# Kernel tuning notes

Measured on AMD Instinct MI355X. Metric: run time of the kernel, lower is better.

Reference implementation:

```python
import jax, jax.numpy as jnp
import numpy as np

B, S, N_NODES, D_IN = 8, 24, 400, 3
D_MODEL = 32
G1_HEADS, G1_DIM = 4, 16
G2_HEADS, G2_DIM = 1, 32
T_KEY = 32


def _ln(x, g, b, eps=1e-6):
    m = jnp.mean(x, -1, keepdims=True)
    v = jnp.var(x, -1, keepdims=True)
    return g * (x - m) / jnp.sqrt(v + eps) + b


def _gat(x, adj, wq, bq, wk, bk, wv, bv, heads, dim):
    # x: [B*, N, F]; adjacency-masked multi-head attention (GraphAttention)
    Bx, N, _ = x.shape
    q = (x @ wq + bq).reshape(Bx, N, heads, dim)
    k = (x @ wk + bk).reshape(Bx, N, heads, dim)
    v = (x @ wv + bv).reshape(Bx, N, heads, dim)
    s = jnp.einsum('bihd,bjhd->bhij', q, k) / jnp.sqrt(jnp.float32(dim))
    s = jnp.where((adj == 0)[None, None], jnp.float32(-1e9), s)
    w = jax.nn.softmax(s, axis=-1)
    o = jnp.einsum('bhij,bjhd->bihd', w, v)
    return o.reshape(Bx, N, heads * dim)


def _mha(x, wq, bq, wk, bk, wv, bv, wo, bo):
    # keras MultiHeadAttention(num_heads=2, key_dim=32), self-attention, output dim = 32
    q = jnp.einsum('bsd,dhk->bshk', x, wq) + bq
    k = jnp.einsum('bsd,dhk->bshk', x, wk) + bk
    v = jnp.einsum('bsd,dhk->bshk', x, wv) + bv
    a = jax.nn.softmax(jnp.einsum('bqhk,bshk->bhqs', q, k) / jnp.sqrt(jnp.float32(T_KEY)), axis=-1)
    o = jnp.einsum('bhqs,bshk->bqhk', a, v)
    return jnp.einsum('bqhk,hko->bqo', o, wo) + bo


def setup_inputs() -> dict:
    ks = jax.random.split(jax.random.key(0), 20)

    def w(k, shape, scale=0.05):
        return (jax.random.normal(k, shape) * scale).astype(jnp.float32)

    z = lambda *s: jnp.zeros(s, jnp.float32)
    one = lambda *s: jnp.ones(s, jnp.float32)

    d = {}
    d['inputs'] = jax.random.normal(ks[0], (B, S, N_NODES, D_IN), dtype=jnp.float32)
    adj = (jax.random.uniform(ks[1], (N_NODES, N_NODES)) < 0.05).astype(jnp.float32)
    adj = jnp.minimum(adj + jnp.eye(N_NODES, dtype=jnp.float32), 1.0)
    d['adj'] = adj / (jnp.sum(adj, axis=1, keepdims=True) + 1e-6)  # row-normalized

    d['g1_wq'] = w(ks[2], (D_IN, G1_HEADS * G1_DIM)); d['g1_bq'] = z(G1_HEADS * G1_DIM)
    d['g1_wk'] = w(ks[3], (D_IN, G1_HEADS * G1_DIM)); d['g1_bk'] = z(G1_HEADS * G1_DIM)
    d['g1_wv'] = w(ks[4], (D_IN, G1_HEADS * G1_DIM)); d['g1_bv'] = z(G1_HEADS * G1_DIM)
    d['g2_wq'] = w(ks[5], (G1_HEADS * G1_DIM, G2_DIM)); d['g2_bq'] = z(G2_DIM)
    d['g2_wk'] = w(ks[6], (G1_HEADS * G1_DIM, G2_DIM)); d['g2_bk'] = z(G2_DIM)
    d['g2_wv'] = w(ks[7], (G1_HEADS * G1_DIM, G2_DIM)); d['g2_bv'] = z(G2_DIM)
    d['sp_g'] = one(D_MODEL); d['sp_b'] = z(D_MODEL)
    d['t_wq'] = w(ks[8], (D_MODEL, 2, T_KEY)); d['t_bq'] = z(2, T_KEY)
    d['t_wk'] = w(ks[9], (D_MODEL, 2, T_KEY)); d['t_bk'] = z(2, T_KEY)
    d['t_wv'] = w(ks[10], (D_MODEL, 2, T_KEY)); d['t_bv'] = z(2, T_KEY)
    d['t_wo'] = w(ks[11], (2, T_KEY, D_MODEL)); d['t_bo'] = z(D_MODEL)
    d['ff_w1'] = w(ks[12], (D_MODEL, 64)); d['ff_b1'] = z(64)
    d['ff_w2'] = w(ks[13], (64, D_MODEL)); d['ff_b2'] = z(D_MODEL)
    d['ln1_g'] = one(D_MODEL); d['ln1_b'] = z(D_MODEL)
    d['ln2_g'] = one(D_MODEL); d['ln2_b'] = z(D_MODEL)
    d['fin_g'] = one(D_MODEL); d['fin_b'] = z(D_MODEL)
    d['fd_w'] = w(ks[14], (D_MODEL, 1), scale=0.01); d['fd_b'] = z(1)
    return d


def reference(inputs, adj, g1_wq, g1_bq, g1_wk, g1_bk, g1_wv, g1_bv,
              g2_wq, g2_bq, g2_wk, g2_bk, g2_wv, g2_bv, sp_g, sp_b,
              t_wq, t_bq, t_wk, t_bk, t_wv, t_bv, t_wo, t_bo,
              ff_w1, ff_b1, ff_w2, ff_b2, ln1_g, ln1_b, ln2_g, ln2_b,
              fin_g, fin_b, fd_w, fd_b):
    Bx, Sx, N, _ = inputs.shape
    x = inputs.reshape(Bx * Sx, N, D_IN)

    # SpatialProcessor: GAT1 -> relu -> GAT2 -> residual layernorm
    h = jax.nn.relu(_gat(x, adj, g1_wq, g1_bq, g1_wk, g1_bk, g1_wv, g1_bv, G1_HEADS, G1_DIM))
    h = _gat(h, adj, g2_wq, g2_bq, g2_wk, g2_bk, g2_wv, g2_bv, G2_HEADS, G2_DIM)
    res = jnp.pad(x, ((0, 0), (0, 0), (0, D_MODEL - D_IN)))  # zero-pad 3 -> 32 for residual
    sp = _ln(h + res, sp_g, sp_b)
    sp4 = sp.reshape(Bx, Sx, N, D_MODEL)  # [B, S, N, 32]

    # TemporalTransformer over sequence per node
    t_in = jnp.transpose(sp4, (0, 2, 1, 3)).reshape(Bx * N, Sx, D_MODEL)
    a = _mha(t_in, t_wq, t_bq, t_wk, t_bk, t_wv, t_bv, t_wo, t_bo)
    x1 = _ln(t_in + a, ln1_g, ln1_b)
    f = jax.nn.gelu(x1 @ ff_w1 + ff_b1, approximate=False) @ ff_w2 + ff_b2
    t_out = _ln(x1 + f, ln2_g, ln2_b).reshape(Bx, N, Sx, D_MODEL)

    # fuse: mean over seq (spatial) + mean over seq (temporal), layernorm, final dense
    fused = _ln(jnp.mean(sp4, axis=1) + jnp.mean(t_out, axis=2), fin_g, fin_b)
    return (fused @ fd_w + fd_b)[..., 0]  # [B, N]
```

## Files before the change

kernel.cpp:

```cpp
#include <hip/hip_runtime.h>
#include <hip/hip_bf16.h>

#define NN 400
#define KMAX 64

struct PtrTable {
  const void* p[36];
  int off[37];
};

__device__ __forceinline__ float bflo(unsigned u) {
  union { unsigned i; float f; } x; x.i = u << 16; return x.f;
}
__device__ __forceinline__ float bfhi(unsigned u) {
  union { unsigned i; float f; } x; x.i = u & 0xffff0000u; return x.f;
}
__device__ __forceinline__ unsigned short f2bf(float f) {
  __hip_bfloat16 b = __float2bfloat16(f);
  return *reinterpret_cast<unsigned short*>(&b);
}
__device__ __forceinline__ unsigned packbf(float a, float b) {
  return (unsigned)f2bf(a) | ((unsigned)f2bf(b) << 16);
}

__global__ void detect_dtype_k(const unsigned short* __restrict__ probe,
                               int* __restrict__ flag) {
  int lane = threadIdx.x;
  unsigned short u = probe[lane * 2];
  int e = (u >> 7) & 0xFF;
  bool plaus = (u == 0) || (e >= 112 && e <= 132);
  unsigned long long m = __ballot(plaus);
  if (lane == 0) flag[0] = (__popcll(m) >= 48) ? 1 : 0;
}

__global__ void convert_k(PtrTable pt, const int* __restrict__ flag,
                          float* __restrict__ dst) {
  bool isbf = flag[0] != 0;
  int total = pt.off[36];
  for (int i = blockIdx.x * blockDim.x + threadIdx.x; i < total;
       i += gridDim.x * blockDim.x) {
    int lo = 0, hi = 35;
    while (lo < hi) {
      int mid = (lo + hi + 1) >> 1;
      if (i >= pt.off[mid]) lo = mid; else hi = mid - 1;
    }
    int rel = i - pt.off[lo];
    float v;
    if (isbf) v = __bfloat162float(((const __hip_bfloat16*)pt.p[lo])[rel]);
    else      v = ((const float*)pt.p[lo])[rel];
    dst[i] = v;
  }
}

__global__ void build_csr_k(const float* __restrict__ adj,
                            int* __restrict__ colp, int* __restrict__ degp) {
  int row = blockIdx.x, lane = threadIdx.x;
  int base = 0;
  for (int j0 = 0; j0 < NN; j0 += 64) {
    int j = j0 + lane;
    bool nz = (j < NN) && (adj[row * NN + j] != 0.0f);
    unsigned long long m = __ballot(nz);
    int offl = __popcll(m & ((1ull << lane) - 1ull));
    if (nz) {
      int pidx = base + offl;
      if (pidx < KMAX) colp[row * KMAX + pidx] = j;
    }
    base += __popcll(m);
  }
  if (lane == 0) degp[row] = base < KMAX ? base : KMAX;
}

__global__ __launch_bounds__(256) void gat1_k(
    const float* __restrict__ xin, const float* __restrict__ g1,
    const int* __restrict__ colp, const int* __restrict__ degp,
    unsigned short* __restrict__ h1b) {
  __shared__ float xs[NN * 3];
  __shared__ float w1s[768];
  __shared__ unsigned short kb[NN * 18];
  __shared__ unsigned short vb[NN * 18];
  const int tid = threadIdx.x;
  const int g = blockIdx.x, co = blockIdx.y * 16;
  for (int e = tid; e < NN * 3; e += 256) xs[e] = xin[g * NN * 3 + e];
  for (int e = tid; e < 768; e += 256) w1s[e] = g1[e];
  __syncthreads();
  for (int e = tid; e < NN * 16; e += 256) {
    int n = e >> 4, c = e & 15;
    float x0 = xs[n * 3], x1 = xs[n * 3 + 1], x2 = xs[n * 3 + 2];
    int wc = co + c;
    float kk = w1s[448 + wc] + x0 * w1s[256 + wc] + x1 * w1s[320 + wc] + x2 * w1s[384 + wc];
    float vv = w1s[704 + wc] + x0 * w1s[512 + wc] + x1 * w1s[576 + wc] + x2 * w1s[640 + wc];
    kb[n * 18 + c] = f2bf(kk);
    vb[n * 18 + c] = f2bf(vv);
  }
  __syncthreads();
  for (int i = tid; i < NN; i += 256) {
    float x0 = xs[i * 3], x1 = xs[i * 3 + 1], x2 = xs[i * 3 + 2];
    float q[16], o[16];
    #pragma unroll
    for (int c = 0; c < 16; ++c) {
      int wc = co + c;
      q[c] = w1s[192 + wc] + x0 * w1s[wc] + x1 * w1s[64 + wc] + x2 * w1s[128 + wc];
      o[c] = 0.f;
    }
    int dg = degp[i];
    const int* cols = colp + i * KMAX;
    float l = 0.f;
    for (int e = 0; e < dg; ++e) {
      int j = cols[e];
      const unsigned* kr = (const unsigned*)(kb + j * 18);
      const unsigned* vr = (const unsigned*)(vb + j * 18);
      float s = 0.f;
      #pragma unroll
      for (int c = 0; c < 8; ++c) {
        unsigned u = kr[c];
        s += q[2 * c] * bflo(u) + q[2 * c + 1] * bfhi(u);
      }
      float p = __expf(s * 0.25f);
      l += p;
      #pragma unroll
      for (int c = 0; c < 8; ++c) {
        unsigned u = vr[c];
        o[2 * c]     += p * bflo(u);
        o[2 * c + 1] += p * bfhi(u);
      }
    }
    float inv = 1.f / l;
    unsigned* hr = (unsigned*)(h1b + ((size_t)g * NN + i) * 64 + co);
    #pragma unroll
    for (int c = 0; c < 8; ++c)
      hr[c] = packbf(fmaxf(o[2 * c] * inv, 0.f), fmaxf(o[2 * c + 1] * inv, 0.f));
  }
}

__global__ __launch_bounds__(256) void gat2_proj_k(
    const unsigned short* __restrict__ h1b, const float* __restrict__ g2,
    unsigned short* __restrict__ q2b, unsigned short* __restrict__ k2g,
    unsigned short* __restrict__ v2g) {
  __shared__ float ht[64 * 65];
  __shared__ float wqs[2048], wks[2048], wvs[2048];
  __shared__ float bqs[32], bks[32], bvs[32];
  const int tid = threadIdx.x, t = blockIdx.x;
  for (int e = tid; e < 2048; e += 256) {
    unsigned u = ((const unsigned*)h1b)[t * 2048 + e];
    int ln = e >> 5, d = (e & 31) * 2;
    ht[ln * 65 + d] = bflo(u);
    ht[ln * 65 + d + 1] = bfhi(u);
  }
  for (int e = tid; e < 2048; e += 256) {
    wqs[e] = g2[e]; wks[e] = g2[2080 + e]; wvs[e] = g2[4160 + e];
  }
  if (tid < 32) { bqs[tid] = g2[2048 + tid]; bks[tid] = g2[4128 + tid]; bvs[tid] = g2[6208 + tid]; }
  __syncthreads();
  const int c = tid & 31, ng = tid >> 5;
  float qa[8], ka[8], va[8];
  #pragma unroll
  for (int k = 0; k < 8; ++k) { qa[k] = bqs[c]; ka[k] = bks[c]; va[k] = bvs[c]; }
  for (int d = 0; d < 64; ++d) {
    float wq = wqs[d * 32 + c], wk = wks[d * 32 + c], wv = wvs[d * 32 + c];
    #pragma unroll
    for (int k = 0; k < 8; ++k) {
      float hv = ht[(ng * 8 + k) * 65 + d];
      qa[k] += hv * wq; ka[k] += hv * wk; va[k] += hv * wv;
    }
  }
  #pragma unroll
  for (int k = 0; k < 8; ++k) {
    int gn = t * 64 + ng * 8 + k;
    q2b[gn * 32 + c] = f2bf(qa[k]);
    k2g[gn * 32 + c] = f2bf(ka[k]);
    v2g[gn * 32 + c] = f2bf(va[k]);
  }
}

__global__ __launch_bounds__(256) void gat2_attn_k(
    const float* __restrict__ xin, const unsigned short* __restrict__ q2b,
    const unsigned short* __restrict__ k2g, const unsigned short* __restrict__ v2g,
    const float* __restrict__ spw, const int* __restrict__ colp,
    const int* __restrict__ degp, float* __restrict__ spo) {
  __shared__ unsigned short k2s[NN * 34];
  __shared__ unsigned short v2s[NN * 34];
  __shared__ float gw[64];
  const int tid = threadIdx.x;
  const int g = blockIdx.x;
  if (tid < 64) gw[tid] = spw[tid];
  for (int e = tid; e < 6400; e += 256) {
    unsigned uk = ((const unsigned*)k2g)[g * 6400 + e];
    unsigned uv = ((const unsigned*)v2g)[g * 6400 + e];
    int n = e >> 4, c = (e & 15) * 2;
    *(unsigned*)(k2s + n * 34 + c) = uk;
    *(unsigned*)(v2s + n * 34 + c) = uv;
  }
  __syncthreads();
  const int b = g / 24, st = g % 24;
  const int i0 = blockIdx.y * 200;
  for (int i = i0 + tid; i < i0 + 200; i += 256) {
    const unsigned* qr = (const unsigned*)(q2b + ((size_t)g * NN + i) * 32);
    float q[32], o[32];
    #pragma unroll
    for (int c = 0; c < 16; ++c) {
      unsigned u = qr[c];
      q[2 * c] = bflo(u); q[2 * c + 1] = bfhi(u);
      o[2 * c] = 0.f; o[2 * c + 1] = 0.f;
    }
    int dg = degp[i];
    const int* cols = colp + i * KMAX;
    float l = 0.f;
    for (int e = 0; e < dg; ++e) {
      int j = cols[e];
      const unsigned* kr = (const unsigned*)(k2s + j * 34);
      float s = 0.f;
      #pragma unroll
      for (int c = 0; c < 16; ++c) {
        unsigned u = kr[c];
        s += q[2 * c] * bflo(u) + q[2 * c + 1] * bfhi(u);
      }
      float p = __expf(s * 0.17677669529663688f);
      l += p;
      const unsigned* vr = (const unsigned*)(v2s + j * 34);
      #pragma unroll
      for (int c = 0; c < 16; ++c) {
        unsigned u = vr[c];
        o[2 * c]     += p * bflo(u);
        o[2 * c + 1] += p * bfhi(u);
      }
    }
    float inv = 1.f / l;
    const float* xr = xin + ((size_t)g * NN + i) * 3;
    float row[32];
    #pragma unroll
    for (int c = 0; c < 32; ++c) row[c] = o[c] * inv;
    row[0] += xr[0]; row[1] += xr[1]; row[2] += xr[2];
    float mean = 0.f;
    #pragma unroll
    for (int c = 0; c < 32; ++c) mean += row[c];
    mean *= (1.f / 32.f);
    float var = 0.f;
    #pragma unroll
    for (int c = 0; c < 32; ++c) { float dd = row[c] - mean; var += dd * dd; }
    var *= (1.f / 32.f);
    float rinv = 1.f / sqrtf(var + 1e-6f);
    float* so = spo + (((size_t)b * NN + i) * 24 + st) * 32;
    float4* so4 = (float4*)so;
    #pragma unroll
    for (int k = 0; k < 8; ++k) {
      float4 v;
      v.x = gw[4 * k]     * (row[4 * k]     - mean) * rinv + gw[32 + 4 * k];
      v.y = gw[4 * k + 1] * (row[4 * k + 1] - mean) * rinv + gw[33 + 4 * k];
      v.z = gw[4 * k + 2] * (row[4 * k + 2] - mean) * rinv + gw[34 + 4 * k];
      v.w = gw[4 * k + 3] * (row[4 * k + 3] - mean) * rinv + gw[35 + 4 * k];
      so4[k] = v;
    }
  }
}

__global__ __launch_bounds__(128) void temporal_k(
    const float* __restrict__ sp, const float* __restrict__ tw,
    const int* __restrict__ flag, void* __restrict__ outp) {
  __shared__ float sm[7472];
  float* t_s = sm;
  float* q_s = sm + 768;
  float* k_s = sm + 2328;
  float* v_s = sm + 3888;
  float* aw  = sm + 5448;
  float* x1s = sm + 6648;
  float* red = sm + 7440;
  float* att = q_s;
  float* f1s = k_s;
  float* tos = v_s;
  const int tid = threadIdx.x;

  const float* twq = tw;            const float* tbq = tw + 2048;
  const float* twk = tw + 2112;     const float* tbk = tw + 4160;
  const float* twv = tw + 4224;     const float* tbv = tw + 6272;
  const float* two = tw + 6336;     const float* tbo = tw + 8384;
  const float* fw1 = tw + 8416;     const float* fb1 = tw + 10464;
  const float* fw2 = tw + 10528;    const float* fb2 = tw + 12576;
  const float* l1g = tw + 12608;    const float* l1b = tw + 12640;
  const float* l2g = tw + 12672;    const float* l2b = tw + 12704;
  const float* fng = tw + 12736;    const float* fnb = tw + 12768;
  const float* fdw = tw + 12800;    const float* fdb = tw + 12832;

  const float4* base4 = (const float4*)(sp + (size_t)blockIdx.x * 768);
  for (int e = tid; e < 192; e += 128) ((float4*)t_s)[e] = base4[e];
  __syncthreads();

  {
    const int hk = tid & 63, sh = tid >> 6;
    for (int a = 0; a < 3; ++a) {
      const float* W  = (a == 0) ? twq : (a == 1) ? twk : twv;
      const float* Bb = (a == 0) ? tbq : (a == 1) ? tbk : tbv;
      float* dst      = (a == 0) ? q_s : (a == 1) ? k_s : v_s;
      float w[32];
      #pragma unroll
      for (int c = 0; c < 32; ++c) w[c] = W[c * 64 + hk];
      float bias = Bb[hk];
      for (int s = sh * 12; s < sh * 12 + 12; ++s) {
        float acc = bias;
        const float* tr = t_s + s * 32;
        #pragma unroll
        for (int c = 0; c < 32; ++c) acc += tr[c] * w[c];
        dst[s * 65 + hk] = acc;
      }
    }
  }
  __syncthreads();

  if (tid < 96) {
    const int h = tid / 48, rem = tid % 48, qs = rem >> 1, half = rem & 1;
    const float* qr = q_s + qs * 65 + h * 32;
    float sc[12], l = 0.f;
    #pragma unroll
    for (int k = 0; k < 12; ++k) {
      const float* kr = k_s + (half * 12 + k) * 65 + h * 32;
      float s = 0.f;
      #pragma unroll
      for (int d = 0; d < 32; ++d) s += qr[d] * kr[d];
      sc[k] = __expf(s * 0.17677669529663688f);
      l += sc[k];
    }
    l += __shfl_xor(l, 1);
    float inv = 1.f / l;
    float* ar = aw + (h * 24 + qs) * 25 + half * 12;
    #pragma unroll
    for (int k = 0; k < 12; ++k) ar[k] = sc[k] * inv;
  }
  __syncthreads();

  for (int e = tid; e < 1536; e += 128) {
    int qs = e >> 6, hk = e & 63, h = hk >> 5;
    const float* ar = aw + (h * 24 + qs) * 25;
    float a = 0.f;
    #pragma unroll
    for (int ss = 0; ss < 24; ++ss) a += ar[ss] * v_s[ss * 65 + hk];
    att[qs * 65 + hk] = a;
  }
  __syncthreads();

  for (int e = tid; e < 768; e += 128) {
    int s = e >> 5, c = e & 31;
    const float* ar = att + s * 65;
    float a = tbo[c];
    #pragma unroll 8
    for (int hk = 0; hk < 64; ++hk) a += ar[hk] * two[hk * 32 + c];
    x1s[s * 33 + c] = t_s[e] + a;
  }
  __syncthreads();
  if (tid < 24) {
    float* r = x1s + tid * 33;
    float mean = 0.f;
    for (int c = 0; c < 32; ++c) mean += r[c];
    mean *= (1.f / 32.f);
    float var = 0.f;
    for (int c = 0; c < 32; ++c) { float d = r[c] - mean; var += d * d; }
    var *= (1.f / 32.f);
    float ri = 1.f / sqrtf(var + 1e-6f);
    for (int c = 0; c < 32; ++c) r[c] = l1g[c] * (r[c] - mean) * ri + l1b[c];
  }
  __syncthreads();

  {
    const int j = tid & 63, sh = tid >> 6;
    float w[32];
    #pragma unroll
    for (int c = 0; c < 32; ++c) w[c] = fw1[c * 64 + j];
    float bias = fb1[j];
    for (int s = sh * 12; s < sh * 12 + 12; ++s) {
      float acc = bias;
      const float* xr = x1s + s * 33;
      #pragma unroll
      for (int c = 0; c < 32; ++c) acc += xr[c] * w[c];
      f1s[s * 64 + j] = 0.5f * acc * (1.f + erff(acc * 0.70710678118654752f));
    }
  }
  __syncthreads();

  for (int e = tid; e < 768; e += 128) {
    int s = e >> 5, c = e & 31;
    const float* fr = f1s + s * 64;
    float a = fb2[c];
    #pragma unroll 8
    for (int j = 0; j < 64; ++j) a += fr[j] * fw2[j * 32 + c];
    tos[s * 33 + c] = x1s[s * 33 + c] + a;
  }
  __syncthreads();
  if (tid < 24) {
    float* r = tos + tid * 33;
    float mean = 0.f;
    for (int c = 0; c < 32; ++c) mean += r[c];
    mean *= (1.f / 32.f);
    float var = 0.f;
    for (int c = 0; c < 32; ++c) { float d = r[c] - mean; var += d * d; }
    var *= (1.f / 32.f);
    float ri = 1.f / sqrtf(var + 1e-6f);
    for (int c = 0; c < 32; ++c) r[c] = l2g[c] * (r[c] - mean) * ri + l2b[c];
  }
  __syncthreads();

  if (tid < 32) {
    float ms = 0.f, mt = 0.f;
    for (int s = 0; s < 24; ++s) { ms += t_s[s * 32 + tid]; mt += tos[s * 33 + tid]; }
    red[tid] = (ms + mt) * (1.f / 24.f);
  }
  __syncthreads();
  if (tid == 0) {
    float mean = 0.f;
    for (int c = 0; c < 32; ++c) mean += red[c];
    mean *= (1.f / 32.f);
    float var = 0.f;
    for (int c = 0; c < 32; ++c) { float d = red[c] - mean; var += d * d; }
    var *= (1.f / 32.f);
    float ri = 1.f / sqrtf(var + 1e-6f);
    float acc = fdb[0];
    for (int c = 0; c < 32; ++c)
      acc += (fng[c] * (red[c] - mean) * ri + fnb[c]) * fdw[c];
    if (flag[0]) ((__hip_bfloat16*)outp)[blockIdx.x] = __float2bfloat16(acc);
    else         ((float*)outp)[blockIdx.x] = acc;
  }
}

extern "C" void kernel_launch(void* const* d_in, const int* in_sizes, int n_in,
                              void* d_out, int out_size, void* d_ws, size_t ws_size,
                              hipStream_t stream) {
  static const int sizes[36] = {
      230400, 160000,
      192, 64, 192, 64, 192, 64,
      2048, 32, 2048, 32, 2048, 32,
      32, 32,
      2048, 64, 2048, 64, 2048, 64, 2048, 32,
      2048, 64, 2048, 32,
      32, 32, 32, 32, 32, 32,
      32, 1};
  PtrTable pt;
  int off = 0;
  for (int i = 0; i < 36; ++i) { pt.p[i] = d_in[i]; pt.off[i] = off; off += sizes[i]; }
  pt.off[36] = off;

  char* ws = (char*)d_ws;
  int*   flag = (int*)ws;
  float* conv = (float*)(ws + 64);
  int*   colp = (int*)(ws + 1835008);
  int*   degp = (int*)(ws + 1937408);
  unsigned short* h1b = (unsigned short*)(ws + 2097152);
  float*          spo = (float*)(ws + 2097152);
  unsigned short* q2b = (unsigned short*)(ws + 11927552);
  unsigned short* k2g = (unsigned short*)(ws + 16842752);
  unsigned short* v2g = (unsigned short*)(ws + 21757952);

  const float* cin  = conv;
  const float* cadj = conv + 230400;
  const float* g1   = conv + 390400;
  const float* g2   = conv + 391168;
  const float* spw  = conv + 397408;
  const float* twp  = conv + 397472;

  hipLaunchKernelGGL(detect_dtype_k, dim3(1), dim3(64), 0, stream,
                     (const unsigned short*)d_in[0], flag);
  hipLaunchKernelGGL(convert_k, dim3(512), dim3(256), 0, stream, pt,
                     (const int*)flag, conv);
  hipLaunchKernelGGL(build_csr_k, dim3(NN), dim3(64), 0, stream, cadj, colp, degp);
  hipLaunchKernelGGL(gat1_k, dim3(192, 4), dim3(256), 0, stream, cin, g1,
                     (const int*)colp, (const int*)degp, h1b);
  hipLaunchKernelGGL(gat2_proj_k, dim3(1200), dim3(256), 0, stream,
                     (const unsigned short*)h1b, g2, q2b, k2g, v2g);
  hipLaunchKernelGGL(gat2_attn_k, dim3(192, 2), dim3(256), 0, stream, cin,
                     (const unsigned short*)q2b, (const unsigned short*)k2g,
                     (const unsigned short*)v2g, spw, (const int*)colp,
                     (const int*)degp, spo);
  hipLaunchKernelGGL(temporal_k, dim3(3200), dim3(128), 0, stream,
                     (const float*)spo, twp, (const int*)flag, d_out);
}
```

Measured before the change: 337.3 us.

## Fold GAT1 projections algebraically, drop input conversion, vectorize temporal and GAT2 kernels

GAT1 now precomputes per-head Wq·Wk^T bilinear coefficients, so attention scores come straight from the 3-dim inputs. Values are aggregated in input space and projected once per node, so the block handles all heads and the grid loses its y dimension. The dtype-detect and full input/adjacency conversion kernels are removed; each kernel probes the dtype inline and reads raw inputs, and only weights are converted. GAT2 projection, GAT2 attention and the temporal kernel get padded, float4-vectorized shared layouts and wave-shuffle layernorm reductions. GAT2 attention now runs as one block per graph instead of two.

```diff
diff --git a/kernel.cpp b/kernel.cpp
--- a/kernel.cpp
+++ b/kernel.cpp
@@ -4,9 +4,9 @@
 #define NN 400
 #define KMAX 64
 
-struct PtrTable {
-  const void* p[36];
-  int off[37];
+struct WTab {
+  const void* p[34];
+  int off[35];
 };
 
 __device__ __forceinline__ float bflo(unsigned u) {
@@ -22,43 +22,48 @@
 __device__ __forceinline__ unsigned packbf(float a, float b) {
   return (unsigned)f2bf(a) | ((unsigned)f2bf(b) << 16);
 }
-
-__global__ void detect_dtype_k(const unsigned short* __restrict__ probe,
-                               int* __restrict__ flag) {
-  int lane = threadIdx.x;
+__device__ __forceinline__ bool detect_bf16(const unsigned short* probe) {
+  int lane = threadIdx.x & 63;
   unsigned short u = probe[lane * 2];
   int e = (u >> 7) & 0xFF;
   bool plaus = (u == 0) || (e >= 112 && e <= 132);
-  unsigned long long m = __ballot(plaus);
-  if (lane == 0) flag[0] = (__popcll(m) >= 48) ? 1 : 0;
-}
-
-__global__ void convert_k(PtrTable pt, const int* __restrict__ flag,
-                          float* __restrict__ dst) {
-  bool isbf = flag[0] != 0;
-  int total = pt.off[36];
+  return __popcll(__ballot(plaus)) >= 48;
+}
+__device__ __forceinline__ float rsum32(float v) {
+  v += __shfl_xor(v, 1); v += __shfl_xor(v, 2); v += __shfl_xor(v, 4);
+  v += __shfl_xor(v, 8); v += __shfl_xor(v, 16); return v;
+}
+
+__global__ void convert_w_k(WTab wt, const unsigned short* __restrict__ probe,
+                            float* __restrict__ dst) {
+  bool isbf = detect_bf16(probe);
+  int total = wt.off[34];
   for (int i = blockIdx.x * blockDim.x + threadIdx.x; i < total;
        i += gridDim.x * blockDim.x) {
-    int lo = 0, hi = 35;
+    int lo = 0, hi = 33;
     while (lo < hi) {
       int mid = (lo + hi + 1) >> 1;
-      if (i >= pt.off[mid]) lo = mid; else hi = mid - 1;
-    }
-    int rel = i - pt.off[lo];
+      if (i >= wt.off[mid]) lo = mid; else hi = mid - 1;
+    }
+    int rel = i - wt.off[lo];
     float v;
-    if (isbf) v = __bfloat162float(((const __hip_bfloat16*)pt.p[lo])[rel]);
-    else      v = ((const float*)pt.p[lo])[rel];
+    if (isbf) v = __bfloat162float(((const __hip_bfloat16*)wt.p[lo])[rel]);
+    else      v = ((const float*)wt.p[lo])[rel];
     dst[i] = v;
   }
 }
 
-__global__ void build_csr_k(const float* __restrict__ adj,
+__global__ void build_csr_k(const void* __restrict__ adj,
+                            const unsigned short* __restrict__ probe,
                             int* __restrict__ colp, int* __restrict__ degp) {
+  bool isbf = detect_bf16(probe);
   int row = blockIdx.x, lane = threadIdx.x;
   int base = 0;
   for (int j0 = 0; j0 < NN; j0 += 64) {
     int j = j0 + lane;
-    bool nz = (j < NN) && (adj[row * NN + j] != 0.0f);
+    bool nz;
+    if (isbf) nz = (j < NN) && ((const unsigned short*)adj)[row * NN + j] != 0;
+    else      nz = (j < NN) && ((const float*)adj)[row * NN + j] != 0.0f;
     unsigned long long m = __ballot(nz);
     int offl = __popcll(m & ((1ull << lane) - 1ull));
     if (nz) {
@@ -71,64 +76,100 @@
 }
 
 __global__ __launch_bounds__(256) void gat1_k(
-    const float* __restrict__ xin, const float* __restrict__ g1,
-    const int* __restrict__ colp, const int* __restrict__ degp,
-    unsigned short* __restrict__ h1b) {
-  __shared__ float xs[NN * 3];
+    const void* __restrict__ xraw, const unsigned short* __restrict__ probe,
+    const float* __restrict__ g1, const int* __restrict__ colp,
+    const int* __restrict__ degp, unsigned short* __restrict__ h1b) {
+  __shared__ float xsf[NN * 4];
+  __shared__ float yhf[4 * NN * 4];
   __shared__ float w1s[768];
-  __shared__ unsigned short kb[NN * 18];
-  __shared__ unsigned short vb[NN * 18];
+  __shared__ float cf[64];
   const int tid = threadIdx.x;
-  const int g = blockIdx.x, co = blockIdx.y * 16;
-  for (int e = tid; e < NN * 3; e += 256) xs[e] = xin[g * NN * 3 + e];
+  const int g = blockIdx.x;
+  bool isbf = detect_bf16(probe);
+
   for (int e = tid; e < 768; e += 256) w1s[e] = g1[e];
-  __syncthreads();
-  for (int e = tid; e < NN * 16; e += 256) {
-    int n = e >> 4, c = e & 15;
-    float x0 = xs[n * 3], x1 = xs[n * 3 + 1], x2 = xs[n * 3 + 2];
-    int wc = co + c;
-    float kk = w1s[448 + wc] + x0 * w1s[256 + wc] + x1 * w1s[320 + wc] + x2 * w1s[384 + wc];
-    float vv = w1s[704 + wc] + x0 * w1s[512 + wc] + x1 * w1s[576 + wc] + x2 * w1s[640 + wc];
-    kb[n * 18 + c] = f2bf(kk);
-    vb[n * 18 + c] = f2bf(vv);
-  }
-  __syncthreads();
+  for (int e = tid; e < NN; e += 256) xsf[e * 4 + 3] = 0.f;
+  for (int e = tid; e < NN * 3; e += 256) {
+    int j = e / 3, a = e - j * 3;
+    float v;
+    if (isbf) v = __bfloat162float(((const __hip_bfloat16*)xraw)[g * NN * 3 + e]);
+    else      v = ((const float*)xraw)[g * NN * 3 + e];
+    xsf[j * 4 + a] = v;
+  }
+  __syncthreads();
+
+  if (tid < 64) {
+    int h = tid >> 4, t = tid & 15, co = h * 16;
+    float acc = 0.f;
+    if (t < 9) {
+      int a = t / 3, b = t - (t / 3) * 3;
+      for (int c = 0; c < 16; ++c) acc += w1s[a * 64 + co + c] * w1s[256 + b * 64 + co + c];
+    } else if (t < 12) {
+      int a = t - 9;
+      for (int c = 0; c < 16; ++c) acc += w1s[a * 64 + co + c] * w1s[448 + co + c];
+    } else if (t < 15) {
+      int b = t - 12;
+      for (int c = 0; c < 16; ++c) acc += w1s[256 + b * 64 + co + c] * w1s[192 + co + c];
+    } else {
+      for (int c = 0; c < 16; ++c) acc += w1s[192 + co + c] * w1s[448 + co + c];
+    }
+    cf[h * 16 + t] = acc;
+  }
+  __syncthreads();
+
+  for (int e = tid; e < NN * 4; e += 256) {
+    int j = e >> 2, h = e & 3;
+    const float* bse = cf + h * 16;
+    float x0 = xsf[j * 4], x1 = xsf[j * 4 + 1], x2 = xsf[j * 4 + 2];
+    float* y = yhf + (h * NN + j) * 4;
+    y[0] = bse[0] * x0 + bse[1] * x1 + bse[2] * x2;
+    y[1] = bse[3] * x0 + bse[4] * x1 + bse[5] * x2;
+    y[2] = bse[6] * x0 + bse[7] * x1 + bse[8] * x2;
+    y[3] = bse[12] * x0 + bse[13] * x1 + bse[14] * x2 + bse[15];
+  }
+  __syncthreads();
+
+  const float4* xs4 = (const float4*)xsf;
+  const float4* yh4 = (const float4*)yhf;
   for (int i = tid; i < NN; i += 256) {
-    float x0 = xs[i * 3], x1 = xs[i * 3 + 1], x2 = xs[i * 3 + 2];
-    float q[16], o[16];
-    #pragma unroll
-    for (int c = 0; c < 16; ++c) {
-      int wc = co + c;
-      q[c] = w1s[192 + wc] + x0 * w1s[wc] + x1 * w1s[64 + wc] + x2 * w1s[128 + wc];
-      o[c] = 0.f;
-    }
+    float4 xi = xs4[i];
+    float ch[4];
+    #pragma unroll
+    for (int h = 0; h < 4; ++h)
+      ch[h] = cf[h * 16 + 9] * xi.x + cf[h * 16 + 10] * xi.y + cf[h * 16 + 11] * xi.z;
+    float l[4] = {0.f, 0.f, 0.f, 0.f};
+    float ax[4], ay[4], az[4];
+    #pragma unroll
+    for (int h = 0; h < 4; ++h) { ax[h] = 0.f; ay[h] = 0.f; az[h] = 0.f; }
     int dg = degp[i];
     const int* cols = colp + i * KMAX;
-    float l = 0.f;
     for (int e = 0; e < dg; ++e) {
       int j = cols[e];
-      const unsigned* kr = (const unsigned*)(kb + j * 18);
-      const unsigned* vr = (const unsigned*)(vb + j * 18);
-      float s = 0.f;
-      #pragma unroll
-      for (int c = 0; c < 8; ++c) {
-        unsigned u = kr[c];
-        s += q[2 * c] * bflo(u) + q[2 * c + 1] * bfhi(u);
-      }
-      float p = __expf(s * 0.25f);
-      l += p;
-      #pragma unroll
-      for (int c = 0; c < 8; ++c) {
-        unsigned u = vr[c];
-        o[2 * c]     += p * bflo(u);
-        o[2 * c + 1] += p * bfhi(u);
-      }
-    }
-    float inv = 1.f / l;
-    unsigned* hr = (unsigned*)(h1b + ((size_t)g * NN + i) * 64 + co);
-    #pragma unroll
-    for (int c = 0; c < 8; ++c)
-      hr[c] = packbf(fmaxf(o[2 * c] * inv, 0.f), fmaxf(o[2 * c + 1] * inv, 0.f));
+      float4 xj = xs4[j];
+      #pragma unroll
+      for (int h = 0; h < 4; ++h) {
+        float4 y = yh4[h * NN + j];
+        float s = (xi.x * y.x + xi.y * y.y + xi.z * y.z + y.w + ch[h]) * 0.25f;
+        float p = __expf(s);
+        l[h] += p;
+        ax[h] += p * xj.x; ay[h] += p * xj.y; az[h] += p * xj.z;
+      }
+    }
+    unsigned* hr = (unsigned*)(h1b + ((size_t)g * NN + i) * 64);
+    #pragma unroll
+    for (int h = 0; h < 4; ++h) {
+      float inv = 1.f / l[h];
+      float b0 = ax[h] * inv, b1 = ay[h] * inv, b2 = az[h] * inv;
+      int co = h * 16;
+      #pragma unroll
+      for (int c = 0; c < 16; c += 2) {
+        float o0 = fmaxf(b0 * w1s[512 + co + c] + b1 * w1s[576 + co + c] +
+                         b2 * w1s[640 + co + c] + w1s[704 + co + c], 0.f);
+        float o1 = fmaxf(b0 * w1s[513 + co + c] + b1 * w1s[577 + co + c] +
+                         b2 * w1s[641 + co + c] + w1s[705 + co + c], 0.f);
+        hr[(co + c) >> 1] = packbf(o0, o1);
+      }
+    }
   }
 }
 
@@ -136,15 +177,15 @@
     const unsigned short* __restrict__ h1b, const float* __restrict__ g2,
     unsigned short* __restrict__ q2b, unsigned short* __restrict__ k2g,
     unsigned short* __restrict__ v2g) {
-  __shared__ float ht[64 * 65];
+  __shared__ float ht[64 * 68];
   __shared__ float wqs[2048], wks[2048], wvs[2048];
   __shared__ float bqs[32], bks[32], bvs[32];
   const int tid = threadIdx.x, t = blockIdx.x;
   for (int e = tid; e < 2048; e += 256) {
     unsigned u = ((const unsigned*)h1b)[t * 2048 + e];
-    int ln = e >> 5, d = (e & 31) * 2;
-    ht[ln * 65 + d] = bflo(u);
-    ht[ln * 65 + d + 1] = bfhi(u);
+    int ln = e >> 5, d0 = (e & 31) * 2;
+    ht[d0 * 68 + ln] = bflo(u);
+    ht[(d0 + 1) * 68 + ln] = bfhi(u);
   }
   for (int e = tid; e < 2048; e += 256) {
     wqs[e] = g2[e]; wks[e] = g2[2080 + e]; wvs[e] = g2[4160 + e];
@@ -157,10 +198,12 @@
   for (int k = 0; k < 8; ++k) { qa[k] = bqs[c]; ka[k] = bks[c]; va[k] = bvs[c]; }
   for (int d = 0; d < 64; ++d) {
     float wq = wqs[d * 32 + c], wk = wks[d * 32 + c], wv = wvs[d * 32 + c];
+    const float4* hp = (const float4*)(ht + d * 68 + ng * 8);
+    float4 h0 = hp[0], h1v = hp[1];
+    float hv[8] = {h0.x, h0.y, h0.z, h0.w, h1v.x, h1v.y, h1v.z, h1v.w};
     #pragma unroll
     for (int k = 0; k < 8; ++k) {
-      float hv = ht[(ng * 8 + k) * 65 + d];
-      qa[k] += hv * wq; ka[k] += hv * wk; va[k] += hv * wv;
+      qa[k] += hv[k] * wq; ka[k] += hv[k] * wk; va[k] += hv[k] * wv;
     }
   }
   #pragma unroll
@@ -173,59 +216,77 @@
 }
 
 __global__ __launch_bounds__(256) void gat2_attn_k(
-    const float* __restrict__ xin, const unsigned short* __restrict__ q2b,
-    const unsigned short* __restrict__ k2g, const unsigned short* __restrict__ v2g,
-    const float* __restrict__ spw, const int* __restrict__ colp,
-    const int* __restrict__ degp, float* __restrict__ spo) {
-  __shared__ unsigned short k2s[NN * 34];
-  __shared__ unsigned short v2s[NN * 34];
+    const void* __restrict__ xraw, const unsigned short* __restrict__ probe,
+    const unsigned short* __restrict__ q2b, const unsigned short* __restrict__ k2g,
+    const unsigned short* __restrict__ v2g, const float* __restrict__ spw,
+    const int* __restrict__ colp, const int* __restrict__ degp,
+    float* __restrict__ spo) {
+  __shared__ unsigned short k2s[NN * 40];
+  __shared__ unsigned short v2s[NN * 40];
   __shared__ float gw[64];
   const int tid = threadIdx.x;
   const int g = blockIdx.x;
+  bool isbf = detect_bf16(probe);
   if (tid < 64) gw[tid] = spw[tid];
   for (int e = tid; e < 6400; e += 256) {
     unsigned uk = ((const unsigned*)k2g)[g * 6400 + e];
     unsigned uv = ((const unsigned*)v2g)[g * 6400 + e];
-    int n = e >> 4, c = (e & 15) * 2;
-    *(unsigned*)(k2s + n * 34 + c) = uk;
-    *(unsigned*)(v2s + n * 34 + c) = uv;
+    int n = e >> 4, c = e & 15;
+    ((unsigned*)k2s)[n * 20 + c] = uk;
+    ((unsigned*)v2s)[n * 20 + c] = uv;
   }
   __syncthreads();
   const int b = g / 24, st = g % 24;
-  const int i0 = blockIdx.y * 200;
-  for (int i = i0 + tid; i < i0 + 200; i += 256) {
-    const unsigned* qr = (const unsigned*)(q2b + ((size_t)g * NN + i) * 32);
+  for (int i = tid; i < NN; i += 256) {
+    const uint4* qp = (const uint4*)(q2b + ((size_t)g * NN + i) * 32);
+    uint4 qw[4] = {qp[0], qp[1], qp[2], qp[3]};
     float q[32], o[32];
     #pragma unroll
-    for (int c = 0; c < 16; ++c) {
-      unsigned u = qr[c];
-      q[2 * c] = bflo(u); q[2 * c + 1] = bfhi(u);
-      o[2 * c] = 0.f; o[2 * c + 1] = 0.f;
-    }
+    for (int t = 0; t < 4; ++t) {
+      unsigned uu[4] = {qw[t].x, qw[t].y, qw[t].z, qw[t].w};
+      #pragma unroll
+      for (int m = 0; m < 4; ++m) {
+        q[t * 8 + 2 * m] = bflo(uu[m]); q[t * 8 + 2 * m + 1] = bfhi(uu[m]);
+      }
+    }
+    #pragma unroll
+    for (int c = 0; c < 32; ++c) o[c] = 0.f;
     int dg = degp[i];
     const int* cols = colp + i * KMAX;
     float l = 0.f;
     for (int e = 0; e < dg; ++e) {
       int j = cols[e];
-      const unsigned* kr = (const unsigned*)(k2s + j * 34);
+      const uint4* kr = (const uint4*)(k2s + j * 40);
+      const uint4* vr = (const uint4*)(v2s + j * 40);
       float s = 0.f;
       #pragma unroll
-      for (int c = 0; c < 16; ++c) {
-        unsigned u = kr[c];
-        s += q[2 * c] * bflo(u) + q[2 * c + 1] * bfhi(u);
+      for (int t = 0; t < 4; ++t) {
+        uint4 kk = kr[t];
+        unsigned uu[4] = {kk.x, kk.y, kk.z, kk.w};
+        #pragma unroll
+        for (int m = 0; m < 4; ++m)
+          s += q[t * 8 + 2 * m] * bflo(uu[m]) + q[t * 8 + 2 * m + 1] * bfhi(uu[m]);
       }
       float p = __expf(s * 0.17677669529663688f);
       l += p;
-      const unsigned* vr = (const unsigned*)(v2s + j * 34);
-      #pragma unroll
-      for (int c = 0; c < 16; ++c) {
-        unsigned u = vr[c];
-        o[2 * c]     += p * bflo(u);
-        o[2 * c + 1] += p * bfhi(u);
+      #pragma unroll
+      for (int t = 0; t < 4; ++t) {
+        uint4 vv = vr[t];
+        unsigned uu[4] = {vv.x, vv.y, vv.z, vv.w};
+        #pragma unroll
+        for (int m = 0; m < 4; ++m) {
+          o[t * 8 + 2 * m]     += p * bflo(uu[m]);
+          o[t * 8 + 2 * m + 1] += p * bfhi(uu[m]);
+        }
       }
     }
     float inv = 1.f / l;
-    const float* xr = xin + ((size_t)g * NN + i) * 3;
+    float xr[3];
+    #pragma unroll
+    for (int a = 0; a < 3; ++a) {
+      if (isbf) xr[a] = __bfloat162float(((const __hip_bfloat16*)xraw)[((size_t)g * NN + i) * 3 + a]);
+      else      xr[a] = ((const float*)xraw)[((size_t)g * NN + i) * 3 + a];
+    }
     float row[32];
     #pragma unroll
     for (int c = 0; c < 32; ++c) row[c] = o[c] * inv;
@@ -239,8 +300,7 @@
     for (int c = 0; c < 32; ++c) { float dd = row[c] - mean; var += dd * dd; }
     var *= (1.f / 32.f);
     float rinv = 1.f / sqrtf(var + 1e-6f);
-    float* so = spo + (((size_t)b * NN + i) * 24 + st) * 32;
-    float4* so4 = (float4*)so;
+    float4* so4 = (float4*)(spo + (((size_t)b * NN + i) * 24 + st) * 32);
     #pragma unroll
     for (int k = 0; k < 8; ++k) {
       float4 v;
@@ -255,19 +315,18 @@
 
 __global__ __launch_bounds__(128) void temporal_k(
     const float* __restrict__ sp, const float* __restrict__ tw,
-    const int* __restrict__ flag, void* __restrict__ outp) {
-  __shared__ float sm[7472];
+    const unsigned short* __restrict__ probe, void* __restrict__ outp) {
+  __shared__ float sm[7728];
   float* t_s = sm;
   float* q_s = sm + 768;
-  float* k_s = sm + 2328;
-  float* v_s = sm + 3888;
-  float* aw  = sm + 5448;
-  float* x1s = sm + 6648;
-  float* red = sm + 7440;
+  float* k_s = sm + 2400;
+  float* v_s = sm + 4032;
+  float* aw  = sm + 5664;
+  float* x1s = sm + 6864;
   float* att = q_s;
   float* f1s = k_s;
-  float* tos = v_s;
   const int tid = threadIdx.x;
+  bool isbf = detect_bf16(probe);
 
   const float* twq = tw;            const float* tbq = tw + 2048;
   const float* twk = tw + 2112;     const float* tbk = tw + 4160;
@@ -286,75 +345,103 @@
 
   {
     const int hk = tid & 63, sh = tid >> 6;
-    for (int a = 0; a < 3; ++a) {
-      const float* W  = (a == 0) ? twq : (a == 1) ? twk : twv;
-      const float* Bb = (a == 0) ? tbq : (a == 1) ? tbk : tbv;
-      float* dst      = (a == 0) ? q_s : (a == 1) ? k_s : v_s;
-      float w[32];
-      #pragma unroll
-      for (int c = 0; c < 32; ++c) w[c] = W[c * 64 + hk];
-      float bias = Bb[hk];
-      for (int s = sh * 12; s < sh * 12 + 12; ++s) {
-        float acc = bias;
-        const float* tr = t_s + s * 32;
+    float wq[32], wk[32], wv[32];
+    #pragma unroll
+    for (int c = 0; c < 32; ++c) {
+      wq[c] = twq[c * 64 + hk]; wk[c] = twk[c * 64 + hk]; wv[c] = twv[c * 64 + hk];
+    }
+    float bq = tbq[hk], bk = tbk[hk], bv = tbv[hk];
+    for (int s = sh * 12; s < sh * 12 + 12; ++s) {
+      const float4* tr4 = (const float4*)(t_s + s * 32);
+      float tt[32];
+      #pragma unroll
+      for (int k = 0; k < 8; ++k) { float4 t4 = tr4[k];
+        tt[4*k] = t4.x; tt[4*k+1] = t4.y; tt[4*k+2] = t4.z; tt[4*k+3] = t4.w; }
+      float qa = bq, ka = bk, va = bv;
+      #pragma unroll
+      for (int c = 0; c < 32; ++c) {
+        qa += tt[c] * wq[c]; ka += tt[c] * wk[c]; va += tt[c] * wv[c];
+      }
+      q_s[s * 68 + hk] = qa; k_s[s * 68 + hk] = ka; v_s[s * 68 + hk] = va;
+    }
+  }
+  __syncthreads();
+
+  {
+    const int h = tid >> 6, l = tid & 63;
+    if (l < 48) {
+      const int qs = l >> 1, half = l & 1;
+      const float4* qr4 = (const float4*)(q_s + qs * 68 + h * 32);
+      float qv[32];
+      #pragma unroll
+      for (int k = 0; k < 8; ++k) { float4 t4 = qr4[k];
+        qv[4*k] = t4.x; qv[4*k+1] = t4.y; qv[4*k+2] = t4.z; qv[4*k+3] = t4.w; }
+      float sc[12], lsum = 0.f;
+      #pragma unroll
+      for (int k = 0; k < 12; ++k) {
+        const float4* kr4 = (const float4*)(k_s + (half * 12 + k) * 68 + h * 32);
+        float s = 0.f;
         #pragma unroll
-        for (int c = 0; c < 32; ++c) acc += tr[c] * w[c];
-        dst[s * 65 + hk] = acc;
-      }
-    }
-  }
-  __syncthreads();
-
-  if (tid < 96) {
-    const int h = tid / 48, rem = tid % 48, qs = rem >> 1, half = rem & 1;
-    const float* qr = q_s + qs * 65 + h * 32;
-    float sc[12], l = 0.f;
-    #pragma unroll
-    for (int k = 0; k < 12; ++k) {
-      const float* kr = k_s + (half * 12 + k) * 65 + h * 32;
-      float s = 0.f;
-      #pragma unroll
-      for (int d = 0; d < 32; ++d) s += qr[d] * kr[d];
-      sc[k] = __expf(s * 0.17677669529663688f);
-      l += sc[k];
-    }
-    l += __shfl_xor(l, 1);
-    float inv = 1.f / l;
-    float* ar = aw + (h * 24 + qs) * 25 + half * 12;
-    #pragma unroll
-    for (int k = 0; k < 12; ++k) ar[k] = sc[k] * inv;
-  }
-  __syncthreads();
-
-  for (int e = tid; e < 1536; e += 128) {
-    int qs = e >> 6, hk = e & 63, h = hk >> 5;
-    const float* ar = aw + (h * 24 + qs) * 25;
-    float a = 0.f;
-    #pragma unroll
-    for (int ss = 0; ss < 24; ++ss) a += ar[ss] * v_s[ss * 65 + hk];
-    att[qs * 65 + hk] = a;
-  }
-  __syncthreads();
-
-  for (int e = tid; e < 768; e += 128) {
-    int s = e >> 5, c = e & 31;
-    const float* ar = att + s * 65;
-    float a = tbo[c];
-    #pragma unroll 8
-    for (int hk = 0; hk < 64; ++hk) a += ar[hk] * two[hk * 32 + c];
-    x1s[s * 33 + c] = t_s[e] + a;
-  }
-  __syncthreads();
-  if (tid < 24) {
-    float* r = x1s + tid * 33;
-    float mean = 0.f;
-    for (int c = 0; c < 32; ++c) mean += r[c];
-    mean *= (1.f / 32.f);
-    float var = 0.f;
-    for (int c = 0; c < 32; ++c) { float d = r[c] - mean; var += d * d; }
-    var *= (1.f / 32.f);
-    float ri = 1.f / sqrtf(var + 1e-6f);
-    for (int c = 0; c < 32; ++c) r[c] = l1g[c] * (r[c] - mean) * ri + l1b[c];
+        for (int m = 0; m < 8; ++m) {
+          float4 kk = kr4[m];
+          s += qv[4*m] * kk.x + qv[4*m+1] * kk.y + qv[4*m+2] * kk.z + qv[4*m+3] * kk.w;
+        }
+        sc[k] = __expf(s * 0.17677669529663688f);
+        lsum += sc[k];
+      }
+      lsum += __shfl_xor(lsum, 1);
+      float inv = 1.f / lsum;
+      float* ar = aw + (h * 24 + qs) * 25 + half * 12;
+      #pragma unroll
+      for (int k = 0; k < 12; ++k) ar[k] = sc[k] * inv;
+    }
+  }
+  __syncthreads();
+
+  {
+    const int g = tid >> 4, hkq = tid & 15, h = hkq >> 3;
+    float4 acc[3];
+    #pragma unroll
+    for (int m = 0; m < 3; ++m) acc[m] = make_float4(0.f, 0.f, 0.f, 0.f);
+    const float4* vs4 = (const float4*)v_s;
+    for (int ss = 0; ss < 24; ++ss) {
+      float4 v4 = vs4[ss * 17 + hkq];
+      #pragma unroll
+      for (int m = 0; m < 3; ++m) {
+        float a = aw[(h * 24 + g + 8 * m) * 25 + ss];
+        acc[m].x += a * v4.x; acc[m].y += a * v4.y;
+        acc[m].z += a * v4.z; acc[m].w += a * v4.w;
+      }
+    }
+    #pragma unroll
+    for (int m = 0; m < 3; ++m) ((float4*)att)[(g + 8 * m) * 17 + hkq] = acc[m];
+  }
+  __syncthreads();
+
+  {
+    const int c = tid & 31, half = (tid >> 5) & 1, w = tid >> 6;
+    float wcol[64];
+    #pragma unroll
+    for (int hk = 0; hk < 64; ++hk) wcol[hk] = two[hk * 32 + c];
+    float bo = tbo[c], g1c = l1g[c], b1c = l1b[c];
+    #pragma unroll
+    for (int k = 0; k < 6; ++k) {
+      int s = (w * 2 + half) + 4 * k;
+      const float4* ar4 = (const float4*)(att + s * 68);
+      float acc = bo;
+      #pragma unroll
+      for (int jj = 0; jj < 16; ++jj) {
+        float4 av = ar4[jj];
+        acc += av.x * wcol[4*jj] + av.y * wcol[4*jj+1] +
+               av.z * wcol[4*jj+2] + av.w * wcol[4*jj+3];
+      }
+      float val = t_s[s * 32 + c] + acc;
+      float mean = rsum32(val) * (1.f / 32.f);
+      float dv = val - mean;
+      float var = rsum32(dv * dv) * (1.f / 32.f);
+      float ri = 1.f / sqrtf(var + 1e-6f);
+      x1s[s * 36 + c] = g1c * dv * ri + b1c;
+    }
   }
   __syncthreads();
 
@@ -365,64 +452,69 @@
     for (int c = 0; c < 32; ++c) w[c] = fw1[c * 64 + j];
     float bias = fb1[j];
     for (int s = sh * 12; s < sh * 12 + 12; ++s) {
+      const float4* xr4 = (const float4*)(x1s + s * 36);
       float acc = bias;
-      const float* xr = x1s + s * 33;
-      #pragma unroll
-      for (int c = 0; c < 32; ++c) acc += xr[c] * w[c];
-      f1s[s * 64 + j] = 0.5f * acc * (1.f + erff(acc * 0.70710678118654752f));
-    }
-  }
-  __syncthreads();
-
-  for (int e = tid; e < 768; e += 128) {
-    int s = e >> 5, c = e & 31;
-    const float* fr = f1s + s * 64;
-    float a = fb2[c];
-    #pragma unroll 8
-    for (int j = 0; j < 64; ++j) a += fr[j] * fw2[j * 32 + c];
-    tos[s * 33 + c] = x1s[s * 33 + c] + a;
-  }
-  __syncthreads();
-  if (tid < 24) {
-    float* r = tos + tid * 33;
-    float mean = 0.f;
-    for (int c = 0; c < 32; ++c) mean += r[c];
-    mean *= (1.f / 32.f);
-    float var = 0.f;
-    for (int c = 0; c < 32; ++c) { float d = r[c] - mean; var += d * d; }
-    var *= (1.f / 32.f);
+      #pragma unroll
+      for (int m = 0; m < 8; ++m) {
+        float4 xv = xr4[m];
+        acc += xv.x * w[4*m] + xv.y * w[4*m+1] + xv.z * w[4*m+2] + xv.w * w[4*m+3];
+      }
+      f1s[s * 68 + j] = 0.5f * acc * (1.f + erff(acc * 0.70710678118654752f));
+    }
+  }
+  __syncthreads();
+
+  {
+    const int c = tid & 31, half = (tid >> 5) & 1, w = tid >> 6;
+    float wcol[64];
+    #pragma unroll
+    for (int j = 0; j < 64; ++j) wcol[j] = fw2[j * 32 + c];
+    float b2 = fb2[c], g2c = l2g[c], b2c = l2b[c];
+    #pragma unroll
+    for (int k = 0; k < 6; ++k) {
+      int s = (w * 2 + half) + 4 * k;
+      const float4* fr4 = (const float4*)(f1s + s * 68);
+      float acc = b2;
+      #pragma unroll
+      for (int jj = 0; jj < 16; ++jj) {
+        float4 fv = fr4[jj];
+        acc += fv.x * wcol[4*jj] + fv.y * wcol[4*jj+1] +
+               fv.z * wcol[4*jj+2] + fv.w * wcol[4*jj+3];
+      }
+      float val = x1s[s * 36 + c] + acc;
+      float mean = rsum32(val) * (1.f / 32.f);
+      float dv = val - mean;
+      float var = rsum32(dv * dv) * (1.f / 32.f);
+      float ri = 1.f / sqrtf(var + 1e-6f);
+      x1s[s * 36 + c] = g2c * dv * ri + b2c;
+    }
+  }
+  __syncthreads();
+
+  if (tid < 32) {
+    const int c = tid;
+    float ms = 0.f, mt = 0.f;
+    #pragma unroll
+    for (int s = 0; s < 24; ++s) { ms += t_s[s * 32 + c]; mt += x1s[s * 36 + c]; }
+    float red = (ms + mt) * (1.f / 24.f);
+    float mean = rsum32(red) * (1.f / 32.f);
+    float dv = red - mean;
+    float var = rsum32(dv * dv) * (1.f / 32.f);
     float ri = 1.f / sqrtf(var + 1e-6f);
-    for (int c = 0; c < 32; ++c) r[c] = l2g[c] * (r[c] - mean) * ri + l2b[c];
-  }
-  __syncthreads();
-
-  if (tid < 32) {
-    float ms = 0.f, mt = 0.f;
-    for (int s = 0; s < 24; ++s) { ms += t_s[s * 32 + tid]; mt += tos[s * 33 + tid]; }
-    red[tid] = (ms + mt) * (1.f / 24.f);
-  }
-  __syncthreads();
-  if (tid == 0) {
-    float mean = 0.f;
-    for (int c = 0; c < 32; ++c) mean += red[c];
-    mean *= (1.f / 32.f);
-    float var = 0.f;
-    for (int c = 0; c < 32; ++c) { float d = red[c] - mean; var += d * d; }
-    var *= (1.f / 32.f);
-    float ri = 1.f / sqrtf(var + 1e-6f);
-    float acc = fdb[0];
-    for (int c = 0; c < 32; ++c)
-      acc += (fng[c] * (red[c] - mean) * ri + fnb[c]) * fdw[c];
-    if (flag[0]) ((__hip_bfloat16*)outp)[blockIdx.x] = __float2bfloat16(acc);
-    else         ((float*)outp)[blockIdx.x] = acc;
+    float y = (fng[c] * dv * ri + fnb[c]) * fdw[c];
+    float tot = rsum32(y);
+    if (c == 0) {
+      float acc = tot + fdb[0];
+      if (isbf) ((__hip_bfloat16*)outp)[blockIdx.x] = __float2bfloat16(acc);
+      else      ((float*)outp)[blockIdx.x] = acc;
+    }
   }
 }
 
 extern "C" void kernel_launch(void* const* d_in, const int* in_sizes, int n_in,
                               void* d_out, int out_size, void* d_ws, size_t ws_size,
                               hipStream_t stream) {
-  static const int sizes[36] = {
-      230400, 160000,
+  static const int wsizes[34] = {
       192, 64, 192, 64, 192, 64,
       2048, 32, 2048, 32, 2048, 32,
       32, 32,
@@ -430,42 +522,38 @@
       2048, 64, 2048, 32,
       32, 32, 32, 32, 32, 32,
       32, 1};
-  PtrTable pt;
+  WTab wt;
   int off = 0;
-  for (int i = 0; i < 36; ++i) { pt.p[i] = d_in[i]; pt.off[i] = off; off += sizes[i]; }
-  pt.off[36] = off;
+  for (int i = 0; i < 34; ++i) { wt.p[i] = d_in[i + 2]; wt.off[i] = off; off += wsizes[i]; }
+  wt.off[34] = off;
 
   char* ws = (char*)d_ws;
-  int*   flag = (int*)ws;
-  float* conv = (float*)(ws + 64);
-  int*   colp = (int*)(ws + 1835008);
-  int*   degp = (int*)(ws + 1937408);
-  unsigned short* h1b = (unsigned short*)(ws + 2097152);
-  float*          spo = (float*)(ws + 2097152);
-  unsigned short* q2b = (unsigned short*)(ws + 11927552);
-  unsigned short* k2g = (unsigned short*)(ws + 16842752);
-  unsigned short* v2g = (unsigned short*)(ws + 21757952);
-
-  const float* cin  = conv;
-  const float* cadj = conv + 230400;
-  const float* g1   = conv + 390400;
-  const float* g2   = conv + 391168;
-  const float* spw  = conv + 397408;
-  const float* twp  = conv + 397472;
-
-  hipLaunchKernelGGL(detect_dtype_k, dim3(1), dim3(64), 0, stream,
-                     (const unsigned short*)d_in[0], flag);
-  hipLaunchKernelGGL(convert_k, dim3(512), dim3(256), 0, stream, pt,
-                     (const int*)flag, conv);
-  hipLaunchKernelGGL(build_csr_k, dim3(NN), dim3(64), 0, stream, cadj, colp, degp);
-  hipLaunchKernelGGL(gat1_k, dim3(192, 4), dim3(256), 0, stream, cin, g1,
+  float* convw = (float*)ws;
+  int*   colp  = (int*)(ws + 81920);
+  int*   degp  = (int*)(ws + 184320);
+  unsigned short* h1b = (unsigned short*)(ws + 196608);
+  float*          spo = (float*)(ws + 196608);
+  unsigned short* q2b = (unsigned short*)(ws + 10027008);
+  unsigned short* k2g = (unsigned short*)(ws + 14942208);
+  unsigned short* v2g = (unsigned short*)(ws + 19857408);
+
+  const float* g1  = convw;
+  const float* g2  = convw + 768;
+  const float* spw = convw + 7008;
+  const float* twp = convw + 7072;
+  const unsigned short* probe = (const unsigned short*)d_in[0];
+
+  hipLaunchKernelGGL(convert_w_k, dim3(40), dim3(256), 0, stream, wt, probe, convw);
+  hipLaunchKernelGGL(build_csr_k, dim3(NN), dim3(64), 0, stream, d_in[1], probe,
+                     colp, degp);
+  hipLaunchKernelGGL(gat1_k, dim3(192), dim3(256), 0, stream, d_in[0], probe, g1,
                      (const int*)colp, (const int*)degp, h1b);
   hipLaunchKernelGGL(gat2_proj_k, dim3(1200), dim3(256), 0, stream,
                      (const unsigned short*)h1b, g2, q2b, k2g, v2g);
-  hipLaunchKernelGGL(gat2_attn_k, dim3(192, 2), dim3(256), 0, stream, cin,
+  hipLaunchKernelGGL(gat2_attn_k, dim3(192), dim3(256), 0, stream, d_in[0], probe,
                      (const unsigned short*)q2b, (const unsigned short*)k2g,
                      (const unsigned short*)v2g, spw, (const int*)colp,
                      (const int*)degp, spo);
   hipLaunchKernelGGL(temporal_k, dim3(3200), dim3(128), 0, stream,
-                     (const float*)spo, twp, (const int*)flag, d_out);
-}
+                     (const float*)spo, twp, probe, d_out);
+}
```

Measured after the change: 359.8 us. +6.7%, slower.
